# Optimization experiments

Hardware: AMD Instinct MI355X
Metric: run time of the kernel (lower is better)

## Reference

```python
import jax, jax.numpy as jnp
import numpy as np

HEAD_DIM = 256
HIDDEN = 1536
INTERMEDIATE = 6144
NUM_KV_HEADS = 1
NUM_Q_HEADS = 8
SCALE = HEAD_DIM ** (-0.5)
PAST_LEN = 8191


def setup_inputs() -> dict:
    key = jax.random.key(0)
    ks = jax.random.split(key, 20)
    def lin(ki, fan_in, fan_out):
        # torch nn.Linear init: U(-1/sqrt(fan_in), 1/sqrt(fan_in)); stored (in, out) for x @ W
        bound = 1.0 / np.sqrt(fan_in)
        W = jax.random.uniform(ki, (fan_in, fan_out), jnp.float32, -bound, bound)
        b = jax.random.uniform(jax.random.fold_in(ki, 1), (fan_out,), jnp.float32, -bound, bound)
        return W, b
    Wq, bq = lin(ks[0], HIDDEN, NUM_Q_HEADS * HEAD_DIM)
    Wk, bk = lin(ks[1], HIDDEN, NUM_KV_HEADS * HEAD_DIM)
    Wv, bv = lin(ks[2], HIDDEN, NUM_KV_HEADS * HEAD_DIM)
    Wo, bo = lin(ks[3], NUM_Q_HEADS * HEAD_DIM, HIDDEN)
    Wg, bg = lin(ks[4], HIDDEN, INTERMEDIATE)
    Wu, bu = lin(ks[5], HIDDEN, INTERMEDIATE)
    Wd, bd = lin(ks[6], INTERMEDIATE, HIDDEN)
    x = jax.random.normal(ks[7], (1, 1, HIDDEN), jnp.float32)
    k_past = jax.random.normal(ks[8], (1, NUM_KV_HEADS, PAST_LEN, HEAD_DIM), jnp.float32)
    v_past = jax.random.normal(ks[9], (1, NUM_KV_HEADS, PAST_LEN, HEAD_DIM), jnp.float32)
    return dict(x=x, k_past=k_past, v_past=v_past,
                Wq=Wq, bq=bq, Wk=Wk, bk=bk, Wv=Wv, bv=bv, Wo=Wo, bo=bo,
                Wg=Wg, bg=bg, Wu=Wu, bu=bu, Wd=Wd, bd=bd)


def reference(x, k_past, v_past, Wq, bq, Wk, bk, Wv, bv, Wo, bo, Wg, bg, Wu, bu, Wd, bd):
    residual = x
    # projections; q: (1, Hq, 1, D), k/v: (1, Hkv, 1, D)
    q = (x @ Wq + bq).reshape(1, 1, NUM_Q_HEADS, HEAD_DIM).transpose(0, 2, 1, 3)
    k = (x @ Wk + bk).reshape(1, 1, NUM_KV_HEADS, HEAD_DIM).transpose(0, 2, 1, 3)
    v = (x @ Wv + bv).reshape(1, 1, NUM_KV_HEADS, HEAD_DIM).transpose(0, 2, 1, 3)
    k_full = jnp.concatenate([k_past, k], axis=2)  # (1, Hkv, S, D)
    v_full = jnp.concatenate([v_past, v], axis=2)
    # GQA: broadcast the single KV head across 8 Q heads (no materialized repeat)
    scores = jnp.einsum('bhqd,bksd->bhqs', q, k_full) * SCALE  # (1, Hq, 1, S)
    attn = jax.nn.softmax(scores, axis=-1)
    out = jnp.einsum('bhqs,bksd->bhqd', attn, v_full)  # (1, Hq, 1, D)
    out = out.transpose(0, 2, 1, 3).reshape(1, 1, NUM_Q_HEADS * HEAD_DIM)
    out = out @ Wo + bo
    x = residual + out
    # MLP: GELU(gate) * up -> down (exact erf GELU, matching torch nn.GELU default)
    ffn = (jax.nn.gelu(x @ Wg + bg, approximate=False) * (x @ Wu + bu)) @ Wd + bd
    return x + ffn
```

## Files before the change

### kernel.cpp

```cpp
#include <hip/hip_runtime.h>
#include <hip/hip_bf16.h>
#include <math.h>

#define PAST 8191
#define SCALEF 0.0625f

using bf = __hip_bfloat16;

__device__ __forceinline__ float bf2f(unsigned short u) {
    return __uint_as_float(((unsigned)u) << 16);
}
__device__ __forceinline__ void unpack8(uint4 r, float* f) {
    f[0] = __uint_as_float(r.x << 16);
    f[1] = __uint_as_float(r.x & 0xffff0000u);
    f[2] = __uint_as_float(r.y << 16);
    f[3] = __uint_as_float(r.y & 0xffff0000u);
    f[4] = __uint_as_float(r.z << 16);
    f[5] = __uint_as_float(r.z & 0xffff0000u);
    f[6] = __uint_as_float(r.w << 16);
    f[7] = __uint_as_float(r.w & 0xffff0000u);
}

template<bool BF16>
__device__ __forceinline__ void load8(const void* W, size_t off, float* f) {
    if constexpr (BF16) {
        uint4 r = *reinterpret_cast<const uint4*>((const unsigned short*)W + off);
        unpack8(r, f);
    } else {
        const float* p = (const float*)W + off;
        float4 a = *reinterpret_cast<const float4*>(p);
        float4 b = *reinterpret_cast<const float4*>(p + 4);
        f[0]=a.x; f[1]=a.y; f[2]=a.z; f[3]=a.w;
        f[4]=b.x; f[5]=b.y; f[6]=b.z; f[7]=b.w;
    }
}
template<bool BF16>
__device__ __forceinline__ void load4(const void* P, size_t off, float* f) {
    if constexpr (BF16) {
        uint2 r = *reinterpret_cast<const uint2*>((const unsigned short*)P + off);
        f[0] = __uint_as_float(r.x << 16); f[1] = __uint_as_float(r.x & 0xffff0000u);
        f[2] = __uint_as_float(r.y << 16); f[3] = __uint_as_float(r.y & 0xffff0000u);
    } else {
        float4 a = *reinterpret_cast<const float4*>((const float*)P + off);
        f[0]=a.x; f[1]=a.y; f[2]=a.z; f[3]=a.w;
    }
}
template<bool BF16>
__device__ __forceinline__ float load1(const void* P, int i) {
    if constexpr (BF16) return bf2f(((const unsigned short*)P)[i]);
    else return ((const float*)P)[i];
}

__global__ __launch_bounds__(256) void probe_kernel(const unsigned int* __restrict__ xw,
                                                    int* __restrict__ flag) {
    __shared__ int cnt;
    if (threadIdx.x == 0) cnt = 0;
    __syncthreads();
    int ok = 0;
    for (int i = threadIdx.x; i < 768; i += 256) {
        unsigned e = (xw[i] >> 7) & 0xff;
        if (e >= 96 && e <= 142) ok++;
    }
    atomicAdd(&cnt, ok);
    __syncthreads();
    if (threadIdx.x == 0) *flag = (cnt > 500) ? 1 : 0;
}

template<bool BF16>
__device__ void qkv_body(const void* x, const void* Wq, const void* bq,
                         const void* Wk, const void* bk, const void* Wv, const void* bv,
                         float* qkv) {
    __shared__ float xs[64];
    int tid = threadIdx.x;
    int i0 = blockIdx.y * 64;
    xs[tid] = load1<BF16>(x, i0 + tid);
    __syncthreads();
    int j = blockIdx.x * 512 + tid * 8;
    const void* W; const void* bias; int stride, jl;
    if (j < 2048)      { W = Wq; bias = bq; stride = 2048; jl = j; }
    else if (j < 2304) { W = Wk; bias = bk; stride = 256;  jl = j - 2048; }
    else               { W = Wv; bias = bv; stride = 256;  jl = j - 2304; }
    float acc[8] = {0,0,0,0,0,0,0,0};
    #pragma unroll 4
    for (int i = 0; i < 64; ++i) {
        float f[8];
        load8<BF16>(W, (size_t)(i0 + i) * stride + jl, f);
        float xv = xs[i];
        #pragma unroll
        for (int q = 0; q < 8; ++q) acc[q] = fmaf(xv, f[q], acc[q]);
    }
    #pragma unroll
    for (int q = 0; q < 8; ++q) atomicAdd(&qkv[j + q], acc[q]);
    if (blockIdx.y == 0) {
        #pragma unroll
        for (int q = 0; q < 8; ++q) atomicAdd(&qkv[j + q], load1<BF16>(bias, jl + q));
    }
}
__global__ __launch_bounds__(64) void qkv_kernel(
    const void* x, const void* Wq, const void* bq, const void* Wk, const void* bk,
    const void* Wv, const void* bv, float* qkv, const int* flag) {
    if (*flag) qkv_body<true>(x, Wq, bq, Wk, bk, Wv, bv, qkv);
    else       qkv_body<false>(x, Wq, bq, Wk, bk, Wv, bv, qkv);
}

template<bool BF16>
__device__ void scores_body(const float* qkv, const void* k_past, float* s) {
    int wave = threadIdx.x >> 6, lane = threadIdx.x & 63;
    int p = blockIdx.x * 4 + wave;
    int d0 = lane * 4;
    float kf[4];
    if (p < PAST) {
        load4<BF16>(k_past, (size_t)p * 256 + d0, kf);
    } else {
        kf[0] = qkv[2048 + d0];     kf[1] = qkv[2048 + d0 + 1];
        kf[2] = qkv[2048 + d0 + 2]; kf[3] = qkv[2048 + d0 + 3];
    }
    float part[8];
    #pragma unroll
    for (int h = 0; h < 8; ++h) {
        const float* qh = qkv + h * 256 + d0;
        part[h] = qh[0]*kf[0] + qh[1]*kf[1] + qh[2]*kf[2] + qh[3]*kf[3];
    }
    #pragma unroll
    for (int m = 1; m < 64; m <<= 1) {
        #pragma unroll
        for (int h = 0; h < 8; ++h) part[h] += __shfl_xor(part[h], m, 64);
    }
    if (lane == 0) {
        #pragma unroll
        for (int h = 0; h < 8; ++h) s[h * 8192 + p] = part[h] * SCALEF;
    }
}
__global__ __launch_bounds__(256) void scores_kernel(
    const float* qkv, const void* k_past, float* s, const int* flag) {
    if (*flag) scores_body<true>(qkv, k_past, s);
    else       scores_body<false>(qkv, k_past, s);
}

__global__ __launch_bounds__(256) void softmax_kernel(
    const float* __restrict__ s, float* __restrict__ a) {
    __shared__ float red[256];
    int h = blockIdx.x, tid = threadIdx.x;
    const float* sh = s + h * 8192;
    float m = -1e30f;
    for (int p = tid; p < 8192; p += 256) m = fmaxf(m, sh[p]);
    red[tid] = m; __syncthreads();
    for (int w = 128; w > 0; w >>= 1) {
        if (tid < w) red[tid] = fmaxf(red[tid], red[tid + w]);
        __syncthreads();
    }
    m = red[0]; __syncthreads();
    float l = 0.f;
    for (int p = tid; p < 8192; p += 256) l += expf(sh[p] - m);
    red[tid] = l; __syncthreads();
    for (int w = 128; w > 0; w >>= 1) {
        if (tid < w) red[tid] += red[tid + w];
        __syncthreads();
    }
    float inv = 1.0f / red[0];
    for (int p = tid; p < 8192; p += 256) a[h * 8192 + p] = expf(sh[p] - m) * inv;
}

template<bool BF16>
__device__ void pv_body(const float* a, const void* v_past, const float* qkv, float* part) {
    __shared__ float red[3 * 2048];
    int wave = threadIdx.x >> 6, lane = threadIdx.x & 63;
    int d0 = lane * 4;
    float o[8][4];
    #pragma unroll
    for (int h = 0; h < 8; ++h)
        #pragma unroll
        for (int r = 0; r < 4; ++r) o[h][r] = 0.f;
    int base = blockIdx.x * 128;
    for (int it = 0; it < 32; ++it) {
        int p = base + wave + it * 4;
        float vf[4];
        if (p < PAST) {
            load4<BF16>(v_past, (size_t)p * 256 + d0, vf);
        } else {
            vf[0] = qkv[2304 + d0];     vf[1] = qkv[2304 + d0 + 1];
            vf[2] = qkv[2304 + d0 + 2]; vf[3] = qkv[2304 + d0 + 3];
        }
        #pragma unroll
        for (int h = 0; h < 8; ++h) {
            float w = a[h * 8192 + p];
            #pragma unroll
            for (int r = 0; r < 4; ++r) o[h][r] = fmaf(w, vf[r], o[h][r]);
        }
    }
    if (wave > 0) {
        float* dst = red + (wave - 1) * 2048;
        #pragma unroll
        for (int h = 0; h < 8; ++h)
            #pragma unroll
            for (int r = 0; r < 4; ++r) dst[h * 256 + d0 + r] = o[h][r];
    }
    __syncthreads();
    if (wave == 0) {
        #pragma unroll
        for (int h = 0; h < 8; ++h)
            #pragma unroll
            for (int r = 0; r < 4; ++r) {
                float v = o[h][r] + red[h*256 + d0 + r] + red[2048 + h*256 + d0 + r]
                        + red[4096 + h*256 + d0 + r];
                part[(size_t)blockIdx.x * 2048 + h * 256 + d0 + r] = v;
            }
    }
}
__global__ __launch_bounds__(256) void pv_kernel(
    const float* a, const void* v_past, const float* qkv, float* part, const int* flag) {
    if (*flag) pv_body<true>(a, v_past, qkv, part);
    else       pv_body<false>(a, v_past, qkv, part);
}

template<bool BF16>
__device__ void oproj_body(const float* part, const void* Wo, const void* bo,
                           const void* xin, float* x2) {
    __shared__ float xs[128];
    int tid = threadIdx.x;
    int i0 = blockIdx.y * 128;
    for (int t = tid; t < 128; t += 64) {
        float sum = 0.f;
        for (int b = 0; b < 64; ++b) sum += part[(size_t)b * 2048 + i0 + t];
        xs[t] = sum;
    }
    __syncthreads();
    int j = blockIdx.x * 512 + tid * 8;
    float acc[8] = {0,0,0,0,0,0,0,0};
    #pragma unroll 4
    for (int i = 0; i < 128; ++i) {
        float f[8];
        load8<BF16>(Wo, (size_t)(i0 + i) * 1536 + j, f);
        float xv = xs[i];
        #pragma unroll
        for (int q = 0; q < 8; ++q) acc[q] = fmaf(xv, f[q], acc[q]);
    }
    #pragma unroll
    for (int q = 0; q < 8; ++q) atomicAdd(&x2[j + q], acc[q]);
    if (blockIdx.y == 0) {
        #pragma unroll
        for (int q = 0; q < 8; ++q)
            atomicAdd(&x2[j + q], load1<BF16>(bo, j + q) + load1<BF16>(xin, j + q));
    }
}
__global__ __launch_bounds__(64) void oproj_kernel(
    const float* part, const void* Wo, const void* bo, const void* xin,
    float* x2, const int* flag) {
    if (*flag) oproj_body<true>(part, Wo, bo, xin, x2);
    else       oproj_body<false>(part, Wo, bo, xin, x2);
}

template<bool BF16>
__device__ void gateup_body(const float* x2, const void* Wg, const void* Wu,
                            float* gacc, float* uacc) {
    __shared__ float xs[128];
    int tid = threadIdx.x; int i0 = blockIdx.y * 128;
    for (int t = tid; t < 128; t += 64) xs[t] = x2[i0 + t];
    __syncthreads();
    const void* W = blockIdx.z ? Wu : Wg;
    float* acc = blockIdx.z ? uacc : gacc;
    int j = blockIdx.x * 512 + tid * 8;
    float a[8] = {0,0,0,0,0,0,0,0};
    #pragma unroll 4
    for (int i = 0; i < 128; ++i) {
        float f[8];
        load8<BF16>(W, (size_t)(i0 + i) * 6144 + j, f);
        float xv = xs[i];
        #pragma unroll
        for (int q = 0; q < 8; ++q) a[q] = fmaf(xv, f[q], a[q]);
    }
    #pragma unroll
    for (int q = 0; q < 8; ++q) atomicAdd(&acc[j + q], a[q]);
}
__global__ __launch_bounds__(64) void gateup_kernel(
    const float* x2, const void* Wg, const void* Wu, float* gacc, float* uacc,
    const int* flag) {
    if (*flag) gateup_body<true>(x2, Wg, Wu, gacc, uacc);
    else       gateup_body<false>(x2, Wg, Wu, gacc, uacc);
}

template<bool BF16>
__device__ void down_body(const float* gacc, const float* uacc, const void* bg,
                          const void* bu, const void* Wd, float* yacc) {
    __shared__ float xs[128];
    int tid = threadIdx.x; int i0 = blockIdx.y * 128;
    for (int t = tid; t < 128; t += 64) {
        int i = i0 + t;
        float g = gacc[i] + load1<BF16>(bg, i);
        float u = uacc[i] + load1<BF16>(bu, i);
        float ge = 0.5f * g * (1.0f + erff(g * 0.70710678118654752f));
        xs[t] = ge * u;
    }
    __syncthreads();
    int j = blockIdx.x * 512 + tid * 8;
    float a[8] = {0,0,0,0,0,0,0,0};
    #pragma unroll 4
    for (int i = 0; i < 128; ++i) {
        float f[8];
        load8<BF16>(Wd, (size_t)(i0 + i) * 1536 + j, f);
        float xv = xs[i];
        #pragma unroll
        for (int q = 0; q < 8; ++q) a[q] = fmaf(xv, f[q], a[q]);
    }
    #pragma unroll
    for (int q = 0; q < 8; ++q) atomicAdd(&yacc[j + q], a[q]);
}
__global__ __launch_bounds__(64) void down_kernel(
    const float* gacc, const float* uacc, const void* bg, const void* bu,
    const void* Wd, float* yacc, const int* flag) {
    if (*flag) down_body<true>(gacc, uacc, bg, bu, Wd, yacc);
    else       down_body<false>(gacc, uacc, bg, bu, Wd, yacc);
}

__global__ __launch_bounds__(256) void final_kernel(
    const float* __restrict__ x2, const float* __restrict__ yacc,
    const void* __restrict__ bd, void* __restrict__ out, const int* __restrict__ flag) {
    int j = blockIdx.x * 256 + threadIdx.x;
    if (j < 1536) {
        int isbf = *flag;
        float b = isbf ? bf2f(((const unsigned short*)bd)[j]) : ((const float*)bd)[j];
        float v = x2[j] + yacc[j] + b;
        if (isbf) ((bf*)out)[j] = __float2bfloat16(v);
        else      ((float*)out)[j] = v;
    }
}

extern "C" void kernel_launch(void* const* d_in, const int* in_sizes, int n_in,
                              void* d_out, int out_size, void* d_ws, size_t ws_size,
                              hipStream_t stream) {
    const void* x  = d_in[0];
    const void* kp = d_in[1];
    const void* vp = d_in[2];
    const void* Wq = d_in[3];
    const void* bq = d_in[4];
    const void* Wk = d_in[5];
    const void* bk = d_in[6];
    const void* Wv = d_in[7];
    const void* bv = d_in[8];
    const void* Wo = d_in[9];
    const void* bo = d_in[10];
    const void* Wg = d_in[11];
    const void* bg = d_in[12];
    const void* Wu = d_in[13];
    const void* bu = d_in[14];
    const void* Wd = d_in[15];
    const void* bd = d_in[16];

    float* ws   = (float*)d_ws;
    float* qkv  = ws;
    float* x2   = ws + 2560;
    float* gacc = ws + 4096;
    float* uacc = ws + 10240;
    float* yacc = ws + 16384;
    float* sc   = ws + 17920;
    float* at   = ws + 83456;
    float* part = ws + 148992;
    int*  flag  = (int*)(ws + 280064);

    hipMemsetAsync(ws, 0, 17920 * sizeof(float), stream);
    probe_kernel<<<1, 256, 0, stream>>>((const unsigned int*)x, flag);

    qkv_kernel<<<dim3(5, 24), 64, 0, stream>>>(x, Wq, bq, Wk, bk, Wv, bv, qkv, flag);
    scores_kernel<<<2048, 256, 0, stream>>>(qkv, kp, sc, flag);
    softmax_kernel<<<8, 256, 0, stream>>>(sc, at);
    pv_kernel<<<64, 256, 0, stream>>>(at, vp, qkv, part, flag);
    oproj_kernel<<<dim3(3, 16), 64, 0, stream>>>(part, Wo, bo, x, x2, flag);
    gateup_kernel<<<dim3(12, 12, 2), 64, 0, stream>>>(x2, Wg, Wu, gacc, uacc, flag);
    down_kernel<<<dim3(3, 48), 64, 0, stream>>>(gacc, uacc, bg, bu, Wd, yacc, flag);
    final_kernel<<<6, 256, 0, stream>>>(x2, yacc, bd, d_out, flag);
}
```

Measured before the change: 314.4 us.

## Fuse scores/softmax/PV into split-K flash kernel and replace atomics with partial buffers

Merges the scores, softmax and PV kernels into one flash-decoding kernel per 128-position chunk that keeps local max and sum, then rescales the partials inside the o-projection kernel. All atomicAdd accumulations and the workspace memset are replaced by per-split partial buffers that the next kernel reduces, with the K-split made finer (64 rows). This removes two launches, the score and probability round trips through global memory, and atomic contention. In exchange, each consumer does redundant partial reductions and more partial data is written and read.

```diff
diff --git a/kernel.cpp b/kernel.cpp
--- a/kernel.cpp
+++ b/kernel.cpp
@@ -67,19 +67,18 @@
 }
 
 template<bool BF16>
-__device__ void qkv_body(const void* x, const void* Wq, const void* bq,
-                         const void* Wk, const void* bk, const void* Wv, const void* bv,
-                         float* qkv) {
+__device__ void qkv_body(const void* x, const void* Wq, const void* Wk,
+                         const void* Wv, float* qkvpart) {
     __shared__ float xs[64];
-    int tid = threadIdx.x;
+    int t = threadIdx.x;
     int i0 = blockIdx.y * 64;
-    xs[tid] = load1<BF16>(x, i0 + tid);
-    __syncthreads();
-    int j = blockIdx.x * 512 + tid * 8;
-    const void* W; const void* bias; int stride, jl;
-    if (j < 2048)      { W = Wq; bias = bq; stride = 2048; jl = j; }
-    else if (j < 2304) { W = Wk; bias = bk; stride = 256;  jl = j - 2048; }
-    else               { W = Wv; bias = bv; stride = 256;  jl = j - 2304; }
+    xs[t] = load1<BF16>(x, i0 + t);
+    __syncthreads();
+    int j = blockIdx.x * 512 + t * 8;
+    const void* W; int stride, jl;
+    if (j < 2048)      { W = Wq; stride = 2048; jl = j; }
+    else if (j < 2304) { W = Wk; stride = 256;  jl = j - 2048; }
+    else               { W = Wv; stride = 256;  jl = j - 2304; }
     float acc[8] = {0,0,0,0,0,0,0,0};
     #pragma unroll 4
     for (int i = 0; i < 64; ++i) {
@@ -89,240 +88,300 @@
         #pragma unroll
         for (int q = 0; q < 8; ++q) acc[q] = fmaf(xv, f[q], acc[q]);
     }
-    #pragma unroll
-    for (int q = 0; q < 8; ++q) atomicAdd(&qkv[j + q], acc[q]);
-    if (blockIdx.y == 0) {
-        #pragma unroll
-        for (int q = 0; q < 8; ++q) atomicAdd(&qkv[j + q], load1<BF16>(bias, jl + q));
-    }
+    float* dst = qkvpart + (size_t)blockIdx.y * 2560 + j;
+    #pragma unroll
+    for (int q = 0; q < 8; ++q) dst[q] = acc[q];
 }
 __global__ __launch_bounds__(64) void qkv_kernel(
-    const void* x, const void* Wq, const void* bq, const void* Wk, const void* bk,
-    const void* Wv, const void* bv, float* qkv, const int* flag) {
-    if (*flag) qkv_body<true>(x, Wq, bq, Wk, bk, Wv, bv, qkv);
-    else       qkv_body<false>(x, Wq, bq, Wk, bk, Wv, bv, qkv);
-}
-
-template<bool BF16>
-__device__ void scores_body(const float* qkv, const void* k_past, float* s) {
-    int wave = threadIdx.x >> 6, lane = threadIdx.x & 63;
-    int p = blockIdx.x * 4 + wave;
-    int d0 = lane * 4;
-    float kf[4];
-    if (p < PAST) {
-        load4<BF16>(k_past, (size_t)p * 256 + d0, kf);
-    } else {
-        kf[0] = qkv[2048 + d0];     kf[1] = qkv[2048 + d0 + 1];
-        kf[2] = qkv[2048 + d0 + 2]; kf[3] = qkv[2048 + d0 + 3];
-    }
-    float part[8];
-    #pragma unroll
-    for (int h = 0; h < 8; ++h) {
-        const float* qh = qkv + h * 256 + d0;
-        part[h] = qh[0]*kf[0] + qh[1]*kf[1] + qh[2]*kf[2] + qh[3]*kf[3];
-    }
-    #pragma unroll
-    for (int m = 1; m < 64; m <<= 1) {
-        #pragma unroll
-        for (int h = 0; h < 8; ++h) part[h] += __shfl_xor(part[h], m, 64);
-    }
-    if (lane == 0) {
-        #pragma unroll
-        for (int h = 0; h < 8; ++h) s[h * 8192 + p] = part[h] * SCALEF;
-    }
-}
-__global__ __launch_bounds__(256) void scores_kernel(
-    const float* qkv, const void* k_past, float* s, const int* flag) {
-    if (*flag) scores_body<true>(qkv, k_past, s);
-    else       scores_body<false>(qkv, k_past, s);
-}
-
-__global__ __launch_bounds__(256) void softmax_kernel(
-    const float* __restrict__ s, float* __restrict__ a) {
-    __shared__ float red[256];
-    int h = blockIdx.x, tid = threadIdx.x;
-    const float* sh = s + h * 8192;
-    float m = -1e30f;
-    for (int p = tid; p < 8192; p += 256) m = fmaxf(m, sh[p]);
-    red[tid] = m; __syncthreads();
-    for (int w = 128; w > 0; w >>= 1) {
-        if (tid < w) red[tid] = fmaxf(red[tid], red[tid + w]);
-        __syncthreads();
-    }
-    m = red[0]; __syncthreads();
-    float l = 0.f;
-    for (int p = tid; p < 8192; p += 256) l += expf(sh[p] - m);
-    red[tid] = l; __syncthreads();
-    for (int w = 128; w > 0; w >>= 1) {
-        if (tid < w) red[tid] += red[tid + w];
-        __syncthreads();
-    }
-    float inv = 1.0f / red[0];
-    for (int p = tid; p < 8192; p += 256) a[h * 8192 + p] = expf(sh[p] - m) * inv;
-}
-
-template<bool BF16>
-__device__ void pv_body(const float* a, const void* v_past, const float* qkv, float* part) {
+    const void* x, const void* Wq, const void* Wk, const void* Wv,
+    float* qkvpart, const int* flag) {
+    if (*flag) qkv_body<true>(x, Wq, Wk, Wv, qkvpart);
+    else       qkv_body<false>(x, Wq, Wk, Wv, qkvpart);
+}
+
+template<bool BF16>
+__device__ void flash_body(const float* qkvpart, const void* bq, const void* bk,
+                           const void* bv, const void* k_past, const void* v_past,
+                           float* opart, float* mg, float* lg) {
+    __shared__ float q_s[2048];
+    __shared__ float kv_new[512];
+    __shared__ float s_tile[8][128];
     __shared__ float red[3 * 2048];
-    int wave = threadIdx.x >> 6, lane = threadIdx.x & 63;
-    int d0 = lane * 4;
+    int tid = threadIdx.x, w = tid >> 6, l = tid & 63;
+
+    for (int j = tid; j < 2048; j += 256) {
+        float s = 0.f;
+        #pragma unroll 4
+        for (int c = 0; c < 24; ++c) s += qkvpart[c * 2560 + j];
+        q_s[j] = s + load1<BF16>(bq, j);
+    }
+    for (int j = tid; j < 512; j += 256) {
+        float s = 0.f;
+        #pragma unroll 4
+        for (int c = 0; c < 24; ++c) s += qkvpart[c * 2560 + 2048 + j];
+        s += (j < 256) ? load1<BF16>(bk, j) : load1<BF16>(bv, j - 256);
+        kv_new[j] = s;
+    }
+    __syncthreads();
+
+    int hi = l >> 5, d0 = (l & 31) * 8;
+    float qr[8][8];
+    #pragma unroll
+    for (int h = 0; h < 8; ++h)
+        #pragma unroll
+        for (int r = 0; r < 8; ++r) qr[h][r] = q_s[h * 256 + d0 + r];
+
+    int base = blockIdx.x * 128;
+    for (int it = 0; it < 16; ++it) {
+        int ploc = w * 32 + it * 2 + hi;
+        int p = base + ploc;
+        float kf[8];
+        if (p < PAST) {
+            load8<BF16>(k_past, (size_t)p * 256 + d0, kf);
+        } else {
+            #pragma unroll
+            for (int r = 0; r < 8; ++r) kf[r] = kv_new[d0 + r];
+        }
+        #pragma unroll
+        for (int h = 0; h < 8; ++h) {
+            float s = 0.f;
+            #pragma unroll
+            for (int r = 0; r < 8; ++r) s = fmaf(qr[h][r], kf[r], s);
+            s += __shfl_xor(s, 1, 64);
+            s += __shfl_xor(s, 2, 64);
+            s += __shfl_xor(s, 4, 64);
+            s += __shfl_xor(s, 8, 64);
+            s += __shfl_xor(s, 16, 64);
+            if ((l & 31) == 0) s_tile[h][ploc] = s * SCALEF;
+        }
+    }
+    __syncthreads();
+
+    {
+        int h = tid >> 5, ii = tid & 31;
+        float v[4];
+        #pragma unroll
+        for (int r = 0; r < 4; ++r) v[r] = s_tile[h][ii + 32 * r];
+        float m = fmaxf(fmaxf(v[0], v[1]), fmaxf(v[2], v[3]));
+        m = fmaxf(m, __shfl_xor(m, 1, 64));
+        m = fmaxf(m, __shfl_xor(m, 2, 64));
+        m = fmaxf(m, __shfl_xor(m, 4, 64));
+        m = fmaxf(m, __shfl_xor(m, 8, 64));
+        m = fmaxf(m, __shfl_xor(m, 16, 64));
+        float e[4], ls = 0.f;
+        #pragma unroll
+        for (int r = 0; r < 4; ++r) { e[r] = expf(v[r] - m); ls += e[r]; }
+        ls += __shfl_xor(ls, 1, 64);
+        ls += __shfl_xor(ls, 2, 64);
+        ls += __shfl_xor(ls, 4, 64);
+        ls += __shfl_xor(ls, 8, 64);
+        ls += __shfl_xor(ls, 16, 64);
+        #pragma unroll
+        for (int r = 0; r < 4; ++r) s_tile[h][ii + 32 * r] = e[r];
+        if (ii == 0) { mg[blockIdx.x * 8 + h] = m; lg[blockIdx.x * 8 + h] = ls; }
+    }
+    __syncthreads();
+
+    int d0p = l * 4;
     float o[8][4];
     #pragma unroll
     for (int h = 0; h < 8; ++h)
         #pragma unroll
         for (int r = 0; r < 4; ++r) o[h][r] = 0.f;
-    int base = blockIdx.x * 128;
     for (int it = 0; it < 32; ++it) {
-        int p = base + wave + it * 4;
+        int ploc = w + it * 4;
+        int p = base + ploc;
         float vf[4];
         if (p < PAST) {
-            load4<BF16>(v_past, (size_t)p * 256 + d0, vf);
+            load4<BF16>(v_past, (size_t)p * 256 + d0p, vf);
         } else {
-            vf[0] = qkv[2304 + d0];     vf[1] = qkv[2304 + d0 + 1];
-            vf[2] = qkv[2304 + d0 + 2]; vf[3] = qkv[2304 + d0 + 3];
+            #pragma unroll
+            for (int r = 0; r < 4; ++r) vf[r] = kv_new[256 + d0p + r];
         }
         #pragma unroll
         for (int h = 0; h < 8; ++h) {
-            float w = a[h * 8192 + p];
-            #pragma unroll
-            for (int r = 0; r < 4; ++r) o[h][r] = fmaf(w, vf[r], o[h][r]);
+            float ph = s_tile[h][ploc];
+            #pragma unroll
+            for (int r = 0; r < 4; ++r) o[h][r] = fmaf(ph, vf[r], o[h][r]);
         }
     }
-    if (wave > 0) {
-        float* dst = red + (wave - 1) * 2048;
+    if (w > 0) {
+        float* dst = red + (w - 1) * 2048;
         #pragma unroll
         for (int h = 0; h < 8; ++h)
             #pragma unroll
-            for (int r = 0; r < 4; ++r) dst[h * 256 + d0 + r] = o[h][r];
-    }
-    __syncthreads();
-    if (wave == 0) {
+            for (int r = 0; r < 4; ++r) dst[h * 256 + d0p + r] = o[h][r];
+    }
+    __syncthreads();
+    if (w == 0) {
         #pragma unroll
         for (int h = 0; h < 8; ++h)
             #pragma unroll
             for (int r = 0; r < 4; ++r) {
-                float v = o[h][r] + red[h*256 + d0 + r] + red[2048 + h*256 + d0 + r]
-                        + red[4096 + h*256 + d0 + r];
-                part[(size_t)blockIdx.x * 2048 + h * 256 + d0 + r] = v;
+                float v = o[h][r] + red[h*256 + d0p + r] + red[2048 + h*256 + d0p + r]
+                        + red[4096 + h*256 + d0p + r];
+                opart[(size_t)blockIdx.x * 2048 + h * 256 + d0p + r] = v;
             }
     }
 }
-__global__ __launch_bounds__(256) void pv_kernel(
-    const float* a, const void* v_past, const float* qkv, float* part, const int* flag) {
-    if (*flag) pv_body<true>(a, v_past, qkv, part);
-    else       pv_body<false>(a, v_past, qkv, part);
-}
-
-template<bool BF16>
-__device__ void oproj_body(const float* part, const void* Wo, const void* bo,
-                           const void* xin, float* x2) {
-    __shared__ float xs[128];
-    int tid = threadIdx.x;
-    int i0 = blockIdx.y * 128;
-    for (int t = tid; t < 128; t += 64) {
-        float sum = 0.f;
-        for (int b = 0; b < 64; ++b) sum += part[(size_t)b * 2048 + i0 + t];
-        xs[t] = sum;
-    }
-    __syncthreads();
-    int j = blockIdx.x * 512 + tid * 8;
+__global__ __launch_bounds__(256) void flash_kernel(
+    const float* qkvpart, const void* bq, const void* bk, const void* bv,
+    const void* k_past, const void* v_past,
+    float* opart, float* mg, float* lg, const int* flag) {
+    if (*flag) flash_body<true>(qkvpart, bq, bk, bv, k_past, v_past, opart, mg, lg);
+    else       flash_body<false>(qkvpart, bq, bk, bv, k_past, v_past, opart, mg, lg);
+}
+
+template<bool BF16>
+__device__ void oproj_body(const float* opart, const float* mg, const float* lg,
+                           const void* Wo, float* x2part) {
+    __shared__ float coef[64];
+    __shared__ float xs[64];
+    int t = threadIdx.x;
+    int i0 = blockIdx.y * 64;
+    int h = i0 >> 8;
+    float mt = mg[t * 8 + h];
+    float M = mt;
+    M = fmaxf(M, __shfl_xor(M, 1, 64));
+    M = fmaxf(M, __shfl_xor(M, 2, 64));
+    M = fmaxf(M, __shfl_xor(M, 4, 64));
+    M = fmaxf(M, __shfl_xor(M, 8, 64));
+    M = fmaxf(M, __shfl_xor(M, 16, 64));
+    M = fmaxf(M, __shfl_xor(M, 32, 64));
+    float c = expf(mt - M);
+    float den = lg[t * 8 + h] * c;
+    den += __shfl_xor(den, 1, 64);
+    den += __shfl_xor(den, 2, 64);
+    den += __shfl_xor(den, 4, 64);
+    den += __shfl_xor(den, 8, 64);
+    den += __shfl_xor(den, 16, 64);
+    den += __shfl_xor(den, 32, 64);
+    coef[t] = c;
+    __syncthreads();
+    int i = i0 + t;
+    float num = 0.f;
+    #pragma unroll 4
+    for (int b = 0; b < 64; ++b) num = fmaf(coef[b], opart[(size_t)b * 2048 + i], num);
+    xs[t] = num / den;
+    __syncthreads();
+    int j = blockIdx.x * 512 + t * 8;
     float acc[8] = {0,0,0,0,0,0,0,0};
     #pragma unroll 4
-    for (int i = 0; i < 128; ++i) {
+    for (int k = 0; k < 64; ++k) {
         float f[8];
-        load8<BF16>(Wo, (size_t)(i0 + i) * 1536 + j, f);
-        float xv = xs[i];
+        load8<BF16>(Wo, (size_t)(i0 + k) * 1536 + j, f);
+        float xv = xs[k];
         #pragma unroll
         for (int q = 0; q < 8; ++q) acc[q] = fmaf(xv, f[q], acc[q]);
     }
-    #pragma unroll
-    for (int q = 0; q < 8; ++q) atomicAdd(&x2[j + q], acc[q]);
-    if (blockIdx.y == 0) {
-        #pragma unroll
-        for (int q = 0; q < 8; ++q)
-            atomicAdd(&x2[j + q], load1<BF16>(bo, j + q) + load1<BF16>(xin, j + q));
-    }
+    float* dst = x2part + (size_t)blockIdx.y * 1536 + j;
+    #pragma unroll
+    for (int q = 0; q < 8; ++q) dst[q] = acc[q];
 }
 __global__ __launch_bounds__(64) void oproj_kernel(
-    const float* part, const void* Wo, const void* bo, const void* xin,
-    float* x2, const int* flag) {
-    if (*flag) oproj_body<true>(part, Wo, bo, xin, x2);
-    else       oproj_body<false>(part, Wo, bo, xin, x2);
-}
-
-template<bool BF16>
-__device__ void gateup_body(const float* x2, const void* Wg, const void* Wu,
-                            float* gacc, float* uacc) {
-    __shared__ float xs[128];
-    int tid = threadIdx.x; int i0 = blockIdx.y * 128;
-    for (int t = tid; t < 128; t += 64) xs[t] = x2[i0 + t];
+    const float* opart, const float* mg, const float* lg, const void* Wo,
+    float* x2part, const int* flag) {
+    if (*flag) oproj_body<true>(opart, mg, lg, Wo, x2part);
+    else       oproj_body<false>(opart, mg, lg, Wo, x2part);
+}
+
+template<bool BF16>
+__device__ void gateup_body(const float* x2part, const void* bo, const void* x,
+                            const void* Wg, const void* Wu, float* gupart) {
+    __shared__ float xs[64];
+    int t = threadIdx.x;
+    int i0 = blockIdx.y * 64;
+    int i = i0 + t;
+    float s = 0.f;
+    #pragma unroll 4
+    for (int c = 0; c < 32; ++c) s += x2part[c * 1536 + i];
+    xs[t] = s + load1<BF16>(bo, i) + load1<BF16>(x, i);
     __syncthreads();
     const void* W = blockIdx.z ? Wu : Wg;
-    float* acc = blockIdx.z ? uacc : gacc;
-    int j = blockIdx.x * 512 + tid * 8;
-    float a[8] = {0,0,0,0,0,0,0,0};
-    #pragma unroll 4
-    for (int i = 0; i < 128; ++i) {
+    int j = blockIdx.x * 512 + t * 8;
+    float acc[8] = {0,0,0,0,0,0,0,0};
+    #pragma unroll 4
+    for (int k = 0; k < 64; ++k) {
         float f[8];
-        load8<BF16>(W, (size_t)(i0 + i) * 6144 + j, f);
-        float xv = xs[i];
-        #pragma unroll
-        for (int q = 0; q < 8; ++q) a[q] = fmaf(xv, f[q], a[q]);
-    }
-    #pragma unroll
-    for (int q = 0; q < 8; ++q) atomicAdd(&acc[j + q], a[q]);
+        load8<BF16>(W, (size_t)(i0 + k) * 6144 + j, f);
+        float xv = xs[k];
+        #pragma unroll
+        for (int q = 0; q < 8; ++q) acc[q] = fmaf(xv, f[q], acc[q]);
+    }
+    float* dst = gupart + ((size_t)blockIdx.z * 24 + blockIdx.y) * 6144 + j;
+    #pragma unroll
+    for (int q = 0; q < 8; ++q) dst[q] = acc[q];
 }
 __global__ __launch_bounds__(64) void gateup_kernel(
-    const float* x2, const void* Wg, const void* Wu, float* gacc, float* uacc,
-    const int* flag) {
-    if (*flag) gateup_body<true>(x2, Wg, Wu, gacc, uacc);
-    else       gateup_body<false>(x2, Wg, Wu, gacc, uacc);
-}
-
-template<bool BF16>
-__device__ void down_body(const float* gacc, const float* uacc, const void* bg,
-                          const void* bu, const void* Wd, float* yacc) {
-    __shared__ float xs[128];
-    int tid = threadIdx.x; int i0 = blockIdx.y * 128;
-    for (int t = tid; t < 128; t += 64) {
-        int i = i0 + t;
-        float g = gacc[i] + load1<BF16>(bg, i);
-        float u = uacc[i] + load1<BF16>(bu, i);
-        float ge = 0.5f * g * (1.0f + erff(g * 0.70710678118654752f));
-        xs[t] = ge * u;
-    }
-    __syncthreads();
-    int j = blockIdx.x * 512 + tid * 8;
-    float a[8] = {0,0,0,0,0,0,0,0};
-    #pragma unroll 4
-    for (int i = 0; i < 128; ++i) {
+    const float* x2part, const void* bo, const void* x,
+    const void* Wg, const void* Wu, float* gupart, const int* flag) {
+    if (*flag) gateup_body<true>(x2part, bo, x, Wg, Wu, gupart);
+    else       gateup_body<false>(x2part, bo, x, Wg, Wu, gupart);
+}
+
+template<bool BF16>
+__device__ void down_body(const float* gupart, const void* bg, const void* bu,
+                          const void* Wd, float* dpart) {
+    __shared__ float xs[64];
+    int t = threadIdx.x;
+    int i0 = blockIdx.y * 64;
+    int i = i0 + t;
+    float g = 0.f, u = 0.f;
+    #pragma unroll 4
+    for (int c = 0; c < 24; ++c) {
+        g += gupart[c * 6144 + i];
+        u += gupart[(24 + c) * 6144 + i];
+    }
+    g += load1<BF16>(bg, i); u += load1<BF16>(bu, i);
+    float ge = 0.5f * g * (1.0f + erff(g * 0.70710678118654752f));
+    xs[t] = ge * u;
+    __syncthreads();
+    int j = blockIdx.x * 512 + t * 8;
+    float acc[8] = {0,0,0,0,0,0,0,0};
+    #pragma unroll 4
+    for (int k = 0; k < 64; ++k) {
         float f[8];
-        load8<BF16>(Wd, (size_t)(i0 + i) * 1536 + j, f);
-        float xv = xs[i];
-        #pragma unroll
-        for (int q = 0; q < 8; ++q) a[q] = fmaf(xv, f[q], a[q]);
-    }
-    #pragma unroll
-    for (int q = 0; q < 8; ++q) atomicAdd(&yacc[j + q], a[q]);
+        load8<BF16>(Wd, (size_t)(i0 + k) * 1536 + j, f);
+        float xv = xs[k];
+        #pragma unroll
+        for (int q = 0; q < 8; ++q) acc[q] = fmaf(xv, f[q], acc[q]);
+    }
+    float* dst = dpart + (size_t)blockIdx.y * 1536 + j;
+    #pragma unroll
+    for (int q = 0; q < 8; ++q) dst[q] = acc[q];
 }
 __global__ __launch_bounds__(64) void down_kernel(
-    const float* gacc, const float* uacc, const void* bg, const void* bu,
-    const void* Wd, float* yacc, const int* flag) {
-    if (*flag) down_body<true>(gacc, uacc, bg, bu, Wd, yacc);
-    else       down_body<false>(gacc, uacc, bg, bu, Wd, yacc);
-}
-
-__global__ __launch_bounds__(256) void final_kernel(
-    const float* __restrict__ x2, const float* __restrict__ yacc,
+    const float* gupart, const void* bg, const void* bu, const void* Wd,
+    float* dpart, const int* flag) {
+    if (*flag) down_body<true>(gupart, bg, bu, Wd, dpart);
+    else       down_body<false>(gupart, bg, bu, Wd, dpart);
+}
+
+__global__ __launch_bounds__(64) void final_kernel(
+    const float* __restrict__ x2part, const float* __restrict__ dpart,
+    const void* __restrict__ bo, const void* __restrict__ x,
     const void* __restrict__ bd, void* __restrict__ out, const int* __restrict__ flag) {
-    int j = blockIdx.x * 256 + threadIdx.x;
-    if (j < 1536) {
-        int isbf = *flag;
-        float b = isbf ? bf2f(((const unsigned short*)bd)[j]) : ((const float*)bd)[j];
-        float v = x2[j] + yacc[j] + b;
-        if (isbf) ((bf*)out)[j] = __float2bfloat16(v);
-        else      ((float*)out)[j] = v;
-    }
+    int j = blockIdx.x * 64 + threadIdx.x;
+    int isbf = *flag;
+    float x2 = 0.f;
+    #pragma unroll 4
+    for (int c = 0; c < 32; ++c) x2 += x2part[c * 1536 + j];
+    float y = 0.f;
+    #pragma unroll 4
+    for (int c = 0; c < 96; ++c) y += dpart[c * 1536 + j];
+    float bov, xv, bdv;
+    if (isbf) {
+        bov = bf2f(((const unsigned short*)bo)[j]);
+        xv  = bf2f(((const unsigned short*)x)[j]);
+        bdv = bf2f(((const unsigned short*)bd)[j]);
+    } else {
+        bov = ((const float*)bo)[j];
+        xv  = ((const float*)x)[j];
+        bdv = ((const float*)bd)[j];
+    }
+    float v = x2 + bov + xv + y + bdv;
+    if (isbf) ((bf*)out)[j] = __float2bfloat16(v);
+    else      ((float*)out)[j] = v;
 }
 
 extern "C" void kernel_launch(void* const* d_in, const int* in_sizes, int n_in,
@@ -346,26 +405,21 @@
     const void* Wd = d_in[15];
     const void* bd = d_in[16];
 
-    float* ws   = (float*)d_ws;
-    float* qkv  = ws;
-    float* x2   = ws + 2560;
-    float* gacc = ws + 4096;
-    float* uacc = ws + 10240;
-    float* yacc = ws + 16384;
-    float* sc   = ws + 17920;
-    float* at   = ws + 83456;
-    float* part = ws + 148992;
-    int*  flag  = (int*)(ws + 280064);
-
-    hipMemsetAsync(ws, 0, 17920 * sizeof(float), stream);
+    float* ws = (float*)d_ws;
+    float* qkvpart = ws;
+    float* opart   = ws + 61440;
+    float* mg      = ws + 192512;
+    float* lg      = ws + 193024;
+    float* x2part  = ws + 193536;
+    float* gupart  = ws + 242688;
+    float* dpart   = ws + 537600;
+    int*  flag     = (int*)(ws + 685056);
+
     probe_kernel<<<1, 256, 0, stream>>>((const unsigned int*)x, flag);
-
-    qkv_kernel<<<dim3(5, 24), 64, 0, stream>>>(x, Wq, bq, Wk, bk, Wv, bv, qkv, flag);
-    scores_kernel<<<2048, 256, 0, stream>>>(qkv, kp, sc, flag);
-    softmax_kernel<<<8, 256, 0, stream>>>(sc, at);
-    pv_kernel<<<64, 256, 0, stream>>>(at, vp, qkv, part, flag);
-    oproj_kernel<<<dim3(3, 16), 64, 0, stream>>>(part, Wo, bo, x, x2, flag);
-    gateup_kernel<<<dim3(12, 12, 2), 64, 0, stream>>>(x2, Wg, Wu, gacc, uacc, flag);
-    down_kernel<<<dim3(3, 48), 64, 0, stream>>>(gacc, uacc, bg, bu, Wd, yacc, flag);
-    final_kernel<<<6, 256, 0, stream>>>(x2, yacc, bd, d_out, flag);
-}
+    qkv_kernel<<<dim3(5, 24), 64, 0, stream>>>(x, Wq, Wk, Wv, qkvpart, flag);
+    flash_kernel<<<64, 256, 0, stream>>>(qkvpart, bq, bk, bv, kp, vp, opart, mg, lg, flag);
+    oproj_kernel<<<dim3(3, 32), 64, 0, stream>>>(opart, mg, lg, Wo, x2part, flag);
+    gateup_kernel<<<dim3(12, 24, 2), 64, 0, stream>>>(x2part, bo, x, Wg, Wu, gupart, flag);
+    down_kernel<<<dim3(3, 96), 64, 0, stream>>>(gupart, bg, bu, Wd, dpart, flag);
+    final_kernel<<<24, 64, 0, stream>>>(x2part, dpart, bo, x, bd, d_out, flag);
+}
```

Result: slower. 322.9 us (+2.7%).
